# Optimization experiments

Measured on AMD Instinct MI355X. Metric: run time of the kernel, lower is better.

## Reference

```python
import jax, jax.numpy as jnp
import numpy as np

SIGMA_D = 1.0
SCALES = (0.1, 0.2, 0.4)
K_VALUES = (5, 10, 25)  # defaults of get_knn_indices
HIDDEN = 64


def _safe_sqrt(x):
    # sqrt with a tiny floor so diagonal zeros don't produce nan grads;
    # fwd diff vs exact sqrt is <= 1e-6 (only on the zero diagonal).
    return jnp.sqrt(jnp.where(x > 0, x, 1e-12))


def _l2norm(x, eps=1e-12):
    # F.normalize(dim=-1)
    n = jnp.linalg.norm(x, axis=-1, keepdims=True)
    return x / jnp.maximum(n, eps)


def setup_inputs() -> dict:
    key = jax.random.key(0)
    ks = jax.random.split(key, 7)
    B, N = 1, 1024
    S = len(SCALES)
    points = jax.random.normal(ks[0], (B, N, 3), dtype=jnp.float32)
    # torch Linear weights stored as (in, out): y = x @ W + b
    W_rtdie = jax.random.normal(ks[1], (1, HIDDEN), dtype=jnp.float32)
    b_rtdie = jax.random.normal(ks[2], (HIDDEN,), dtype=jnp.float32) * 0.01
    W_mdve = jax.random.normal(ks[3], (2 * S, HIDDEN), dtype=jnp.float32) / np.sqrt(2 * S)
    b_mdve = jax.random.normal(ks[4], (HIDDEN,), dtype=jnp.float32) * 0.01
    W_lgee = jax.random.normal(ks[5], (S, HIDDEN), dtype=jnp.float32) / np.sqrt(S)
    b_lgee = jax.random.normal(ks[6], (HIDDEN,), dtype=jnp.float32) * 0.01
    return {"points": points, "W_rtdie": W_rtdie, "b_rtdie": b_rtdie,
            "W_mdve": W_mdve, "b_mdve": b_mdve, "W_lgee": W_lgee, "b_lgee": b_lgee}


def reference(points, W_rtdie, b_rtdie, W_mdve, b_mdve, W_lgee, b_lgee):
    B, N, _ = points.shape
    # single pairwise distance map reused by every branch (torch recomputes it)
    diff = points[:, :, None, :] - points[:, None, :, :]      # (B,N,N,3)
    d2 = jnp.sum(diff * diff, axis=-1)                         # (B,N,N)
    dist = _safe_sqrt(d2)

    # rtdie: exp(-dist/sigma_d) -> Linear(1,H); computed under no_grad in torch
    # and only sets the output broadcast shape — it does NOT enter the output.

    # mdve: multi-scale density + density-gradient
    scales = jnp.asarray(SCALES, dtype=points.dtype)           # (S,)
    vols = (4.0 / 3.0) * np.pi * scales ** 3                   # (S,)
    within = (dist[..., None] < scales).astype(points.dtype)   # (B,N,N,S)
    density = jnp.sum(within, axis=2) / vols                   # (B,N,S)
    dd = density[:, :, None, :] - density[:, None, :, :]       # (B,N,N,S)
    gradient = _safe_sqrt(jnp.sum(dd * dd, axis=2))            # (B,N,S)
    mdve = _l2norm(jnp.concatenate([density, gradient], axis=-1))  # (B,N,2S)

    # lgee: kNN-distance entropy at multiple k
    ents = []
    for k in K_VALUES:
        kk = min(k, N - 1)
        nd = -jax.lax.top_k(-dist, kk + 1)[0][..., 1:]         # (B,N,k) smallest, drop self
        p = nd / jnp.sum(nd, axis=-1, keepdims=True)
        ents.append(-jnp.sum(p * jnp.log(p + 1e-10), axis=-1))
    lgee = _l2norm(jnp.stack(ents, axis=-1))                   # (B,N,len(K))

    mdve_e = _l2norm(mdve @ W_mdve + b_mdve)                   # (B,N,H)
    lgee_e = _l2norm(lgee @ W_lgee + b_lgee)                   # (B,N,H)
    s = mdve_e + lgee_e
    # expand_as(r_d_embeddings): out[0,i,j,h] = s[0,j,h]  (requires B==1)
    return jnp.broadcast_to(s[:, None, :, :], (B, N, N, HIDDEN))
```

## Files before the change

kernel.cpp:

```cpp
#include <hip/hip_runtime.h>
#include <math.h>

#define NPTS 1024
#define HID 64

typedef float v4f __attribute__((ext_vector_type(4)));

__global__ __launch_bounds__(64) void k_rows(const float* __restrict__ pts,
                                             float* __restrict__ density,
                                             float* __restrict__ ent,
                                             unsigned int* __restrict__ icnt) {
    const int i    = blockIdx.x;
    const int lane = threadIdx.x;

    const float px = pts[i * 3 + 0];
    const float py = pts[i * 3 + 1];
    const float pz = pts[i * 3 + 2];

    float v[16];
    int c0 = 0, c1 = 0, c2 = 0;
    #pragma unroll
    for (int q = 0; q < 16; ++q) {
        const int j = lane + q * 64;
        float dx = __fsub_rn(px, pts[j * 3 + 0]);
        float dy = __fsub_rn(py, pts[j * 3 + 1]);
        float dz = __fsub_rn(pz, pts[j * 3 + 2]);
        float d2 = __fadd_rn(__fadd_rn(__fmul_rn(dx, dx), __fmul_rn(dy, dy)),
                             __fmul_rn(dz, dz));
        float d = __fsqrt_rn(d2 > 0.0f ? d2 : 1e-12f);
        v[q] = d;
        c0 += (d < 0.1f);
        c1 += (d < 0.2f);
        c2 += (d < 0.4f);
    }

    unsigned long long packed = (unsigned long long)c0
                              | ((unsigned long long)c1 << 21)
                              | ((unsigned long long)c2 << 42);
    #pragma unroll
    for (int off = 32; off > 0; off >>= 1) packed += __shfl_xor(packed, off);

    #pragma unroll
    for (int k = 2; k <= 16; k <<= 1) {
        #pragma unroll
        for (int j = k >> 1; j > 0; j >>= 1) {
            #pragma unroll
            for (int r = 0; r < 16; ++r) {
                const int l = r ^ j;
                if (l > r) {
                    const bool up = ((r & k) == 0);
                    float lo = fminf(v[r], v[l]);
                    float hi = fmaxf(v[r], v[l]);
                    v[r] = up ? lo : hi;
                    v[l] = up ? hi : lo;
                }
            }
        }
    }

    float s[32];
    #pragma unroll
    for (int r = 0; r < 16; ++r) { s[r] = v[r]; s[16 + r] = 3.0e38f; }

    #pragma unroll
    for (int step = 1; step < 64; step <<= 1) {
        float o[32];
        #pragma unroll
        for (int r = 0; r < 32; ++r) o[r] = __shfl_xor(s[r], step);
        float m[32];
        #pragma unroll
        for (int r = 0; r < 32; ++r) m[r] = fminf(s[r], o[31 - r]);
        #pragma unroll
        for (int j = 16; j > 0; j >>= 1) {
            #pragma unroll
            for (int r = 0; r < 32; ++r) {
                const int l = r ^ j;
                if (l > r) {
                    float lo = fminf(m[r], m[l]);
                    float hi = fmaxf(m[r], m[l]);
                    m[r] = lo;
                    m[l] = hi;
                }
            }
        }
        #pragma unroll
        for (int r = 0; r < 32; ++r) s[r] = m[r];
    }

    const int kvv[3] = {5, 10, 25};
    float E[3];
    #pragma unroll
    for (int q = 0; q < 3; ++q) {
        const int k = kvv[q];
        float S = 0.0f;
        #pragma unroll
        for (int r = 1; r <= 25; ++r) if (r <= k) S += s[r];
        float Ee = 0.0f;
        #pragma unroll
        for (int r = 1; r <= 25; ++r) if (r <= k) {
            float p = s[r] / S;
            Ee -= p * logf(p + 1e-10f);
        }
        E[q] = Ee;
    }

    if (lane == 0) {
        ent[i * 3 + 0] = E[0];
        ent[i * 3 + 1] = E[1];
        ent[i * 3 + 2] = E[2];
        const float scl[3] = {0.1f, 0.2f, 0.4f};
        unsigned int cc[3] = {(unsigned int)(packed & 0x1FFFFF),
                              (unsigned int)((packed >> 21) & 0x1FFFFF),
                              (unsigned int)(packed >> 42)};
        #pragma unroll
        for (int s2 = 0; s2 < 3; ++s2) {
            float sv  = scl[s2];
            float vol = __fmul_rn((float)(4.0 / 3.0 * M_PI),
                                  __fmul_rn(__fmul_rn(sv, sv), sv));
            density[i * 3 + s2] = (float)cc[s2] / vol;
            icnt[i * 3 + s2] = cc[s2];
        }
    }
}

__global__ __launch_bounds__(256) void k_embed(const float* __restrict__ density,
                                               const float* __restrict__ ent,
                                               const unsigned int* __restrict__ icnt,
                                               const float* __restrict__ Wm,
                                               const float* __restrict__ bm,
                                               const float* __restrict__ Wl,
                                               const float* __restrict__ bl,
                                               float* __restrict__ svec) {
    __shared__ double sS[6];
    const int c    = blockIdx.x;
    const int t    = threadIdx.x;
    const int lane = t & 63;
    const int w    = t >> 6;

    if (w == 0) {
        unsigned int sa0 = 0, sa1 = 0, sa2 = 0, sb0 = 0, sb1 = 0, sb2 = 0;
        #pragma unroll
        for (int r = 0; r < 16; ++r) {
            const int row = lane * 16 + r;
            unsigned int c0 = icnt[row * 3 + 0];
            unsigned int c1 = icnt[row * 3 + 1];
            unsigned int c2 = icnt[row * 3 + 2];
            sa0 += c0; sa1 += c1; sa2 += c2;
            sb0 += c0 * c0; sb1 += c1 * c1; sb2 += c2 * c2;
        }
        #pragma unroll
        for (int off = 32; off > 0; off >>= 1) {
            sa0 += __shfl_xor(sa0, off); sa1 += __shfl_xor(sa1, off);
            sa2 += __shfl_xor(sa2, off); sb0 += __shfl_xor(sb0, off);
            sb1 += __shfl_xor(sb1, off); sb2 += __shfl_xor(sb2, off);
        }
        if (lane == 0) {
            const float scl[3] = {0.1f, 0.2f, 0.4f};
            unsigned int A[3] = {sa0, sa1, sa2};
            unsigned int B[3] = {sb0, sb1, sb2};
            #pragma unroll
            for (int s = 0; s < 3; ++s) {
                float sv   = scl[s];
                float volf = __fmul_rn((float)(4.0 / 3.0 * M_PI),
                                       __fmul_rn(__fmul_rn(sv, sv), sv));
                double vold = (double)volf;
                sS[s]     = (double)A[s] / vold;
                sS[3 + s] = (double)B[s] / (vold * vold);
            }
        }
    }
    __syncthreads();

    double S1[3], S2[3];
    #pragma unroll
    for (int s = 0; s < 3; ++s) { S1[s] = sS[s]; S2[s] = sS[3 + s]; }

    #pragma unroll
    for (int kk = 0; kk < 4; ++kk) {
        const int row = 16 * c + 4 * w + kk;

        float m6[6];
        double nrm6 = 0.0;
        #pragma unroll
        for (int s = 0; s < 3; ++s) {
            float d = density[row * 3 + s];
            m6[s] = d;
            double dd = (double)d;
            double g2 = 1024.0 * dd * dd - 2.0 * dd * S1[s] + S2[s];
            m6[3 + s] = (float)sqrt(g2 > 0.0 ? g2 : 1e-12);
        }
        #pragma unroll
        for (int s = 0; s < 6; ++s) nrm6 += (double)m6[s] * (double)m6[s];
        float inv6 = 1.0f / fmaxf((float)sqrt(nrm6), 1e-12f);
        #pragma unroll
        for (int s = 0; s < 6; ++s) m6[s] *= inv6;

        float l3[3];
        double nrm3 = 0.0;
        #pragma unroll
        for (int s = 0; s < 3; ++s) {
            l3[s] = ent[row * 3 + s];
            nrm3 += (double)l3[s] * (double)l3[s];
        }
        float inv3 = 1.0f / fmaxf((float)sqrt(nrm3), 1e-12f);
        #pragma unroll
        for (int s = 0; s < 3; ++s) l3[s] *= inv3;

        float y = bm[lane];
        #pragma unroll
        for (int s = 0; s < 6; ++s) y += m6[s] * Wm[s * HID + lane];
        float yy = y * y;
        #pragma unroll
        for (int off = 32; off > 0; off >>= 1) yy += __shfl_xor(yy, off);
        y *= 1.0f / fmaxf(sqrtf(yy), 1e-12f);

        float z = bl[lane];
        #pragma unroll
        for (int s = 0; s < 3; ++s) z += l3[s] * Wl[s * HID + lane];
        float zz = z * z;
        #pragma unroll
        for (int off = 32; off > 0; off >>= 1) zz += __shfl_xor(zz, off);
        z *= 1.0f / fmaxf(sqrtf(zz), 1e-12f);

        svec[row * HID + lane] = y + z;
    }
}

__global__ __launch_bounds__(256) void k_bcast(const v4f* __restrict__ s4,
                                               v4f* __restrict__ out) {
    const int total = (NPTS * NPTS * HID) / 4;
    const int mask  = (NPTS * HID) / 4 - 1;
    int idx = blockIdx.x * 256 + threadIdx.x;
    const int stride = gridDim.x * 256;
    for (; idx < total; idx += stride) {
        out[idx] = s4[idx & mask];
    }
}

extern "C" void kernel_launch(void* const* d_in, const int* in_sizes, int n_in,
                              void* d_out, int out_size, void* d_ws, size_t ws_size,
                              hipStream_t stream) {
    const float* pts = (const float*)d_in[0];
    const float* Wm = (const float*)d_in[3];
    const float* bm = (const float*)d_in[4];
    const float* Wl = (const float*)d_in[5];
    const float* bl = (const float*)d_in[6];

    char* ws = (char*)d_ws;
    float*        density = (float*)(ws);
    float*        entv    = (float*)(ws + 12288);
    unsigned int* icnt    = (unsigned int*)(ws + 24576);
    float*        svec    = (float*)(ws + 36864);

    float* out = (float*)d_out;

    hipLaunchKernelGGL(k_rows, dim3(NPTS), dim3(64), 0, stream,
                       pts, density, entv, icnt);
    hipLaunchKernelGGL(k_embed, dim3(64), dim3(256), 0, stream,
                       density, entv, icnt, Wm, bm, Wl, bl, svec);
    hipLaunchKernelGGL(k_bcast, dim3(2048), dim3(256), 0, stream,
                       (const v4f*)svec, (v4f*)out);
}
```

Baseline: 69.80 us.

## Fuse embedding computation into broadcast kernel, keeping rows in LDS

Merges the embedding kernel into the broadcast kernel. Each of 2048 blocks recomputes the 16-row embedding slice for its column chunk, stages it in shared memory, and writes it to 32 output rows. This removes one kernel launch and the global round-trip through the svec workspace. In exchange, the embedding work and the global count reduction are repeated 32 times across blocks, which adds redundant compute before the stores begin.

```diff
diff --git a/kernel.cpp b/kernel.cpp
--- a/kernel.cpp
+++ b/kernel.cpp
@@ -123,16 +123,19 @@
     }
 }
 
-__global__ __launch_bounds__(256) void k_embed(const float* __restrict__ density,
+__global__ __launch_bounds__(256) void k_bcast(const float* __restrict__ density,
                                                const float* __restrict__ ent,
                                                const unsigned int* __restrict__ icnt,
                                                const float* __restrict__ Wm,
                                                const float* __restrict__ bm,
                                                const float* __restrict__ Wl,
                                                const float* __restrict__ bl,
-                                               float* __restrict__ svec) {
+                                               v4f* __restrict__ out) {
+    __shared__ float  s_lds[16 * HID];
     __shared__ double sS[6];
-    const int c    = blockIdx.x;
+    const int b    = blockIdx.x;
+    const int c    = b & 63;
+    const int g    = b >> 6;
     const int t    = threadIdx.x;
     const int lane = t & 63;
     const int w    = t >> 6;
@@ -222,18 +225,17 @@
         for (int off = 32; off > 0; off >>= 1) zz += __shfl_xor(zz, off);
         z *= 1.0f / fmaxf(sqrtf(zz), 1e-12f);
 
-        svec[row * HID + lane] = y + z;
-    }
-}
-
-__global__ __launch_bounds__(256) void k_bcast(const v4f* __restrict__ s4,
-                                               v4f* __restrict__ out) {
-    const int total = (NPTS * NPTS * HID) / 4;
-    const int mask  = (NPTS * HID) / 4 - 1;
-    int idx = blockIdx.x * 256 + threadIdx.x;
-    const int stride = gridDim.x * 256;
-    for (; idx < total; idx += stride) {
-        out[idx] = s4[idx & mask];
+        s_lds[(4 * w + kk) * HID + lane] = y + z;
+    }
+    __syncthreads();
+
+    const v4f val = *(const v4f*)&s_lds[4 * t];
+
+    v4f* dst = out + (size_t)(g * 32) * (NPTS * HID / 4) + c * 256 + t;
+    #pragma unroll 4
+    for (int ii = 0; ii < 32; ++ii) {
+        *dst = val;
+        dst += NPTS * HID / 4;
     }
 }
 
@@ -250,14 +252,11 @@
     float*        density = (float*)(ws);
     float*        entv    = (float*)(ws + 12288);
     unsigned int* icnt    = (unsigned int*)(ws + 24576);
-    float*        svec    = (float*)(ws + 36864);
 
     float* out = (float*)d_out;
 
     hipLaunchKernelGGL(k_rows, dim3(NPTS), dim3(64), 0, stream,
                        pts, density, entv, icnt);
-    hipLaunchKernelGGL(k_embed, dim3(64), dim3(256), 0, stream,
-                       density, entv, icnt, Wm, bm, Wl, bl, svec);
-    hipLaunchKernelGGL(k_bcast, dim3(2048), dim3(256), 0, stream,
-                       (const v4f*)svec, (v4f*)out);
+    hipLaunchKernelGGL(k_bcast, dim3(64 * 32), dim3(256), 0, stream,
+                       density, entv, icnt, Wm, bm, Wl, bl, (v4f*)out);
 }
```

Measured after the change: 68.47 us. No clear change (-1.9%).
